# Kernel tuning notes

Measured on AMD Instinct MI355X. Metric: run time of the kernel, lower is better.

## Reference

```python
import jax, jax.numpy as jnp
import numpy as np

NUM_HEAD = 8
DIM_HEAD = 32
IN_DIM = 256  # = NUM_HEAD * DIM_HEAD
SLEN = 1024
BSZ = 8


def setup_inputs() -> dict:
    key = jax.random.key(0)
    ks = jax.random.split(key, 6)
    std = 1.0 / np.sqrt(DIM_HEAD).astype(np.float32)
    h = jax.random.normal(ks[0], (SLEN, BSZ, IN_DIM), dtype=jnp.float32)
    W_y = std * jax.random.normal(ks[1], (1, NUM_HEAD, DIM_HEAD, DIM_HEAD), dtype=jnp.float32)
    W_q = std * jax.random.normal(ks[2], (1, NUM_HEAD, DIM_HEAD, DIM_HEAD), dtype=jnp.float32)
    W_k = std * jax.random.normal(ks[3], (1, NUM_HEAD, DIM_HEAD, DIM_HEAD), dtype=jnp.float32)
    w_b = std * jax.random.normal(ks[4], (1, NUM_HEAD, DIM_HEAD, 4), dtype=jnp.float32)
    # out_linear: Linear(H*d -> in_dim, bias=False); torch weight shape (in_dim, H*d)
    W_out = jax.random.normal(ks[5], (IN_DIM, NUM_HEAD * DIM_HEAD), dtype=jnp.float32) / np.sqrt(NUM_HEAD * DIM_HEAD).astype(np.float32)
    return {"h": h, "W_y": W_y, "W_q": W_q, "W_k": W_k, "w_b": w_b, "W_out": W_out}


def _read(W, v):
    # W: (B,H,d,d), v: (B,H,d) -> (B,H,d)
    return jnp.einsum('bhij,bhj->bhi', W, v)


def _read_b(wb, v):
    # wb: (B,H,d,4), v: (B,H,d) -> (B,H,4)
    return jnp.einsum('bhik,bhi->bhk', wb, v)


def _srwm_forward(h, W_y, W_q, W_k, w_b, W_out):
    slen, bsz, _ = h.shape
    # reshape to heads and softmax the input (as in the torch forward)
    x = jax.nn.softmax(h.reshape(slen, bsz, NUM_HEAD, DIM_HEAD), axis=-1)  # (S,B,H,d)
    bc = lambda W: jnp.broadcast_to(W, (bsz,) + W.shape[1:])
    carry0 = (bc(W_y), bc(W_q), bc(W_k), bc(w_b))

    def step(carry, xt):
        Wy, Wq, Wk, wb = carry  # (B,H,d,d) x3, (B,H,d,4)
        yt = _read(Wy, xt)                                   # output read with current Wy
        qt = jax.nn.softmax(_read(Wq, xt), axis=-1)          # query
        kt = jax.nn.softmax(_read(Wk, xt), axis=-1)          # key
        bt = jax.nn.sigmoid(_read_b(wb, xt))                 # (B,H,4) learning rates
        # delta-rule self-referential update: W += beta * (W q - W k) (x) k
        dy = _read(Wy, qt) - _read(Wy, kt)
        dq = _read(Wq, qt) - _read(Wq, kt)
        dk = _read(Wk, qt) - _read(Wk, kt)
        db = _read_b(wb, qt) - _read_b(wb, kt)               # (B,H,4)
        outer = lambda u: u[..., :, None] * kt[..., None, :]
        Wy = Wy + bt[..., 0][..., None, None] * outer(dy)
        Wq = Wq + bt[..., 1][..., None, None] * outer(dq)
        Wk = Wk + bt[..., 2][..., None, None] * outer(dk)
        wb = wb + bt[..., 3][..., None, None] * (kt[..., :, None] * db[..., None, :])
        return (Wy, Wq, Wk, wb), yt

    _, ys = jax.lax.scan(step, carry0, x)                    # ys: (S,B,H,d)
    out = ys.reshape(slen, bsz, NUM_HEAD * DIM_HEAD) @ W_out.T  # (S,B,in_dim)
    return h + out  # dropout p=0 -> identity; residual


def reference(h, W_y, W_q, W_k, w_b, W_out):
    return _srwm_forward(h, W_y, W_q, W_k, w_b, W_out)
```

## Files before the change

### kernel.cpp

```cpp
#include <hip/hip_runtime.h>

#define DEV __device__ __forceinline__


template <int CTRL>
DEV float dppf(float x) {
  return __int_as_float(__builtin_amdgcn_update_dpp(
      0, __float_as_int(x), CTRL, 0xF, 0xF, true));
}

DEV float wsum32(float v) {
  v += dppf<0xB1>(v);
  v += dppf<0x4E>(v);
  v += dppf<0x141>(v);
  v += dppf<0x140>(v);
#if __has_builtin(__builtin_amdgcn_permlane16_swap)
  {
    auto p = __builtin_amdgcn_permlane16_swap(
        __float_as_uint(v), __float_as_uint(v), false, false);
    v = __uint_as_float(p[0]) + __uint_as_float(p[1]);
  }
#else
  v += __shfl_xor(v, 16, 64);
#endif
  return v;
}

DEV float halfsum(float v) {
#if __has_builtin(__builtin_amdgcn_permlane32_swap)
  auto p = __builtin_amdgcn_permlane32_swap(
      __float_as_uint(v), __float_as_uint(v), false, false);
  return __uint_as_float(p[0]) + __uint_as_float(p[1]);
#else
  return v + __shfl_xor(v, 32, 64);
#endif
}

#define SLEN 1024
#define NH 8
#define DH 32
#define HSTRIDE 2048


__global__ __launch_bounds__(256)
void srwm_xsm(const float* __restrict__ h, float* __restrict__ x) {
  int i = blockIdx.x * 256 + threadIdx.x;
  float e = __expf(h[i]);
  x[i] = __fdividef(e, wsum32(e));
}


#define BARRIER() \
  do { asm volatile("s_waitcnt lgkmcnt(0)" ::: "memory"); \
       __builtin_amdgcn_s_barrier(); } while (0)

#define REGION(T, P, XS, XP)                                                  \
  {                                                                           \
    \
    float ql[16], kl[16];                                                     \
    _Pragma("unroll") for (int j = 0; j < 16; j += 4) {                       \
      *(float4*)&ql[j] = *(const float4*)&qs[(P) ^ 1][c0 + j];                \
      *(float4*)&kl[j] = *(const float4*)&ks2[(P) ^ 1][c0 + j];               \
    }                                                                         \
    float Bw = bss[(P) ^ 1][w];                                               \
    _Pragma("unroll") for (int j = 0; j < 16; ++j) ql[j] -= kl[j];            \
                   \
    float d0 = 0.f, d1 = 0.f, d2 = 0.f, d3 = 0.f, s0 = 0.f, s1 = 0.f;        \
    _Pragma("unroll") for (int j = 0; j < 16; j += 4) {                       \
      d0 = fmaf(W[j],     ql[j],     d0);                                     \
      d1 = fmaf(W[j + 1], ql[j + 1], d1);                                     \
      d2 = fmaf(W[j + 2], ql[j + 2], d2);                                     \
      d3 = fmaf(W[j + 3], ql[j + 3], d3);                                     \
      s0 = fmaf(kl[j],     XS[j],     s0);                                    \
      s1 = fmaf(kl[j + 1], XS[j + 1], s1);                                    \
      s0 = fmaf(kl[j + 2], XS[j + 2], s0);                                    \
      s1 = fmaf(kl[j + 3], XS[j + 3], s1);                                    \
    }                                                                         \
    float dsum = halfsum((d0 + d1) + (d2 + d3));                              \
    float sv   = halfsum(s0 + s1);                                            \
        \
    int t2 = (T) + 2; if (t2 > SLEN - 1) t2 = SLEN - 1;                       \
    _Pragma("unroll") for (int j = 0; j < 16; j += 4)                         \
      *(float4*)&XS[j] = *(const float4*)(xb + (size_t)t2 * HSTRIDE + c0 + j);\
    float u  = Bw * dsum;                                                     \
    float aA = fmaf(u, sv, preA);                                             \
    if (w == 0) {                                                             \
      if (lane < DH) xb[(size_t)(T) * HSTRIDE + lane] = aA;          \
    } else if (w == 1) {                                                      \
      float e = __expf(aA); float qq = __fdividef(e, wsum32(e));              \
      qs[P][r] = qq;                         \
    } else if (w == 2) {                                                      \
      float e = __expf(aA); float kk2 = __fdividef(e, wsum32(e));             \
      ks2[P][r] = kk2;                                                        \
    } else {                                                                  \
      float sg = __fdividef(1.f, 1.f + __expf(-aA));                          \
      if (lane < 4) bss[P][lane] = sg;                                        \
    }                                                                         \
                                      \
    _Pragma("unroll") for (int j = 0; j < 16; ++j)                            \
      W[j] = fmaf(u, kl[j], W[j]);                                            \
    float p0 = 0.f, p1 = 0.f, p2 = 0.f, p3 = 0.f;                             \
    _Pragma("unroll") for (int j = 0; j < 16; j += 4) {                       \
      p0 = fmaf(W[j],     XP[j],     p0);                                     \
      p1 = fmaf(W[j + 1], XP[j + 1], p1);                                     \
      p2 = fmaf(W[j + 2], XP[j + 2], p2);                                     \
      p3 = fmaf(W[j + 3], XP[j + 3], p3);                                     \
    }                                                                         \
    preA = halfsum((p0 + p1) + (p2 + p3));                                    \
    BARRIER();                                                                \
  }

__global__ __launch_bounds__(256, 1)
void srwm_scan(const float* __restrict__ Wy0, const float* __restrict__ Wq0,
               const float* __restrict__ Wk0, const float* __restrict__ wb0,
               float* xy) {
  __shared__ float qs[2][DH];
  __shared__ float ks2[2][DH];
  __shared__ float bss[2][4];

  const int bh   = blockIdx.x;
  const int hd   = bh & 7;
  const int w    = threadIdx.x >> 6;
  const int lane = threadIdx.x & 63;
  const int r    = lane & 31;
  const int c0   = (lane >> 5) * 16;

  float W[16];
  if (w < 3) {
    const float* src = (w == 0) ? Wy0 : (w == 1) ? Wq0 : Wk0;
    const float* p = src + (hd * DH + r) * DH + c0;
#pragma unroll
    for (int j = 0; j < 16; j += 4) *(float4*)&W[j] = *(const float4*)(p + j);
  } else {
    const int kk = r & 3;
#pragma unroll
    for (int j = 0; j < 16; ++j) W[j] = wb0[(hd * DH + c0 + j) * 4 + kk];
  }

  if (threadIdx.x < DH) { qs[1][threadIdx.x] = 0.f; ks2[1][threadIdx.x] = 0.f; }
  if (threadIdx.x < 4)  { bss[1][threadIdx.x] = 0.f; bss[0][threadIdx.x] = 0.f; }

  float* xb = xy + bh * DH;

  float X0[16], X1[16];
#pragma unroll
  for (int j = 0; j < 16; j += 4) {
    *(float4*)&X0[j] = *(const float4*)(xb + c0 + j);
    *(float4*)&X1[j] = *(const float4*)(xb + HSTRIDE + c0 + j);
  }
  float p0 = 0.f, p1 = 0.f, p2 = 0.f, p3 = 0.f;
#pragma unroll
  for (int j = 0; j < 16; j += 4) {
    p0 = fmaf(W[j],     X0[j],     p0);
    p1 = fmaf(W[j + 1], X0[j + 1], p1);
    p2 = fmaf(W[j + 2], X0[j + 2], p2);
    p3 = fmaf(W[j + 3], X0[j + 3], p3);
  }
  float preA = halfsum((p0 + p1) + (p2 + p3));
  __syncthreads();

  for (int t = 0; t < SLEN; t += 2) {
    REGION(t,     0, X0, X1);
    REGION(t + 1, 1, X1, X0);
  }
}


__global__ __launch_bounds__(256)
void srwm_proj(const float* __restrict__ h, const float* __restrict__ ys,
               const float* __restrict__ Wout, float* __restrict__ out) {
  __shared__ float ytile[32][256];
  const int r0  = blockIdx.x * 32;
  const int tid = threadIdx.x;

  const float4* src = (const float4*)(ys + (size_t)r0 * 256);
  float4*       dst = (float4*)(&ytile[0][0]);
#pragma unroll
  for (int i = 0; i < 8; ++i) dst[tid + i * 256] = src[tid + i * 256];
  __syncthreads();

  float acc[32];
#pragma unroll
  for (int m = 0; m < 32; ++m) acc[m] = 0.f;

  const float* wrow = Wout + (size_t)tid * 256;
  for (int k = 0; k < 256; k += 4) {
    float4 w = *(const float4*)(wrow + k);
#pragma unroll
    for (int m = 0; m < 32; ++m) {
      float4 y4 = *(const float4*)(&ytile[m][k]);
      acc[m] = fmaf(w.x, y4.x,
               fmaf(w.y, y4.y,
               fmaf(w.z, y4.z,
               fmaf(w.w, y4.w, acc[m]))));
    }
  }

#pragma unroll
  for (int m = 0; m < 32; ++m) {
    int row = r0 + m;
    out[(size_t)row * 256 + tid] = h[(size_t)row * 256 + tid] + acc[m];
  }
}


extern "C" void kernel_launch(void* const* d_in, const int* in_sizes, int n_in,
                              void* d_out, int out_size, void* d_ws, size_t ws_size,
                              hipStream_t stream) {
  const float* h    = (const float*)d_in[0];
  const float* Wy0  = (const float*)d_in[1];
  const float* Wq0  = (const float*)d_in[2];
  const float* Wk0  = (const float*)d_in[3];
  const float* wb0  = (const float*)d_in[4];
  const float* Wout = (const float*)d_in[5];
  float* out = (float*)d_out;

  srwm_xsm <<<SLEN * HSTRIDE / 256, 256, 0, stream>>>(h, out);
  srwm_scan<<<64, 256, 0, stream>>>(Wy0, Wq0, Wk0, wb0, out);
  srwm_proj<<<256, 256, 0, stream>>>(h, out, Wout, out);
}
```

Before: 620.4 us.

## Split scan into producer wave for Wq/Wk/wb and consumer wave for Wy

The scan now uses 128 threads. One wave owns Wq, Wk and wb and computes q, k and beta each step. A second wave owns Wy and computes outputs, handing off through an LDS ring buffer with spin-wait counters in place of a block barrier each step. This takes the Wy work and its output stores off the recurrence critical path and drops the per-step s_barrier. It also uses packed v_pk_fma_f32 and ds_bpermute broadcasts. In exchange it relies on volatile LDS spin polling between waves for correctness and loses some parallelism per block.

```diff
diff --git a/kernel.cpp b/kernel.cpp
--- a/kernel.cpp
+++ b/kernel.cpp
@@ -2,6 +2,11 @@
 
 #define DEV __device__ __forceinline__
 
+typedef float f2 __attribute__((ext_vector_type(2)));
+
+DEV void pkfma(f2& acc, f2 a, f2 b) {
+  asm("v_pk_fma_f32 %0, %1, %2, %0" : "+v"(acc) : "v"(a), "v"(b));
+}
 
 template <int CTRL>
 DEV float dppf(float x) {
@@ -36,10 +41,16 @@
 #endif
 }
 
+DEV float rlane(float v, int l) {
+  return __int_as_float(__builtin_amdgcn_readlane(__float_as_int(v), l));
+}
+
 #define SLEN 1024
 #define NH 8
 #define DH 32
 #define HSTRIDE 2048
+#define RING 16
+#define SLOTF 72
 
 
 __global__ __launch_bounds__(256)
@@ -50,73 +61,108 @@
 }
 
 
-#define BARRIER() \
-  do { asm volatile("s_waitcnt lgkmcnt(0)" ::: "memory"); \
-       __builtin_amdgcn_s_barrier(); } while (0)
-
-#define REGION(T, P, XS, XP)                                                  \
+#define LOADX(DST, T)                                                         \
+  { const float* xp_ = xb + (size_t)(T) * HSTRIDE + c0;                       \
+    _Pragma("unroll") for (int q4 = 0; q4 < 4; ++q4) {                        \
+      float4 a_ = *(const float4*)(xp_ + q4 * 4);                             \
+      DST[2*q4] = f2{a_.x, a_.y}; DST[2*q4+1] = f2{a_.z, a_.w}; } }
+
+#define MV3(oq, ok, ob, V)                                                    \
+  { f2 aq0={0,0},aq1={0,0},ak0={0,0},ak1={0,0},ab0={0,0},ab1={0,0};           \
+    _Pragma("unroll") for (int j = 0; j < 8; j += 2) {                        \
+      pkfma(aq0, Wq2[j], V[j]); pkfma(aq1, Wq2[j+1], V[j+1]);                 \
+      pkfma(ak0, Wk2[j], V[j]); pkfma(ak1, Wk2[j+1], V[j+1]);                 \
+      pkfma(ab0, WB2[j], V[j]); pkfma(ab1, WB2[j+1], V[j+1]);                 \
+    }                                                                         \
+    f2 aq_=aq0+aq1, ak_=ak0+ak1, ab_=ab0+ab1;                                 \
+    oq = halfsum(aq_.x+aq_.y); ok = halfsum(ak_.x+ak_.y);                     \
+    ob = halfsum(ab_.x+ab_.y); }
+
+#define PSTEP(T, XC, XO)                                                      \
   {                                                                           \
-    \
-    float ql[16], kl[16];                                                     \
-    _Pragma("unroll") for (int j = 0; j < 16; j += 4) {                       \
-      *(float4*)&ql[j] = *(const float4*)&qs[(P) ^ 1][c0 + j];                \
-      *(float4*)&kl[j] = *(const float4*)&ks2[(P) ^ 1][c0 + j];               \
-    }                                                                         \
-    float Bw = bss[(P) ^ 1][w];                                               \
-    _Pragma("unroll") for (int j = 0; j < 16; ++j) ql[j] -= kl[j];            \
-                   \
-    float d0 = 0.f, d1 = 0.f, d2 = 0.f, d3 = 0.f, s0 = 0.f, s1 = 0.f;        \
-    _Pragma("unroll") for (int j = 0; j < 16; j += 4) {                       \
-      d0 = fmaf(W[j],     ql[j],     d0);                                     \
-      d1 = fmaf(W[j + 1], ql[j + 1], d1);                                     \
-      d2 = fmaf(W[j + 2], ql[j + 2], d2);                                     \
-      d3 = fmaf(W[j + 3], ql[j + 3], d3);                                     \
-      s0 = fmaf(kl[j],     XS[j],     s0);                                    \
-      s1 = fmaf(kl[j + 1], XS[j + 1], s1);                                    \
-      s0 = fmaf(kl[j + 2], XS[j + 2], s0);                                    \
-      s1 = fmaf(kl[j + 3], XS[j + 3], s1);                                    \
-    }                                                                         \
-    float dsum = halfsum((d0 + d1) + (d2 + d3));                              \
-    float sv   = halfsum(s0 + s1);                                            \
-        \
-    int t2 = (T) + 2; if (t2 > SLEN - 1) t2 = SLEN - 1;                       \
-    _Pragma("unroll") for (int j = 0; j < 16; j += 4)                         \
-      *(float4*)&XS[j] = *(const float4*)(xb + (size_t)t2 * HSTRIDE + c0 + j);\
-    float u  = Bw * dsum;                                                     \
-    float aA = fmaf(u, sv, preA);                                             \
-    if (w == 0) {                                                             \
-      if (lane < DH) xb[(size_t)(T) * HSTRIDE + lane] = aA;          \
-    } else if (w == 1) {                                                      \
-      float e = __expf(aA); float qq = __fdividef(e, wsum32(e));              \
-      qs[P][r] = qq;                         \
-    } else if (w == 2) {                                                      \
-      float e = __expf(aA); float kk2 = __fdividef(e, wsum32(e));             \
-      ks2[P][r] = kk2;                                                        \
-    } else {                                                                  \
-      float sg = __fdividef(1.f, 1.f + __expf(-aA));                          \
-      if (lane < 4) bss[P][lane] = sg;                                        \
+    int t2_ = (T) + 2; if (t2_ > SLEN - 1) t2_ = SLEN - 1;                    \
+    LOADX(XO, t2_);                         \
+    float eq_ = __expf(pAq), ek_ = __expf(pAk);                               \
+    float qv_ = __fdividef(eq_, wsum32(eq_));                                 \
+    float kv_ = __fdividef(ek_, wsum32(ek_));                                 \
+    float bs_ = __fdividef(1.f, 1.f + __expf(-pAb));                          \
+    float dvv_ = qv_ - kv_;                                                   \
+    f2 dvc[8], kc[8];                                                         \
+    _Pragma("unroll") for (int j = 0; j < 8; ++j) {                           \
+      f2 td_, tk_;                                                            \
+      td_.x = __int_as_float(__builtin_amdgcn_ds_bpermute(b4 + 8*j,     __float_as_int(dvv_))); \
+      td_.y = __int_as_float(__builtin_amdgcn_ds_bpermute(b4 + 8*j + 4, __float_as_int(dvv_))); \
+      tk_.x = __int_as_float(__builtin_amdgcn_ds_bpermute(b4 + 8*j,     __float_as_int(kv_))); \
+      tk_.y = __int_as_float(__builtin_amdgcn_ds_bpermute(b4 + 8*j + 4, __float_as_int(kv_))); \
+      dvc[j] = td_; kc[j] = tk_;                                              \
+    }                                                                         \
+    float dq_, dk_, db_;                                                      \
+    MV3(dq_, dk_, db_, dvc);                              \
+    float B1_ = rlane(bs_, 1), B2_ = rlane(bs_, 2), B3_ = rlane(bs_, 3);      \
+    float uq_ = B1_ * dq_, uk_ = B2_ * dk_, ub_ = B3_ * db_;                  \
+               \
+    float* sl_ = &ringf[((T) & (RING - 1)) * SLOTF];                          \
+    sl_[r] = dvv_; sl_[DH + r] = kv_;                                         \
+    if (lane == 0) sl_[2 * DH] = bs_;                                         \
+    __builtin_amdgcn_sched_barrier(0);                                        \
+    asm volatile("s_waitcnt lgkmcnt(0)");                                     \
+    __builtin_amdgcn_sched_barrier(0);                                        \
+    *pcv = (T) + 1;                                                           \
+    __builtin_amdgcn_sched_barrier(0);                                        \
+                                                      \
+    f2 uuq_ = f2{uq_, uq_}, uuk_ = f2{uk_, uk_}, uub_ = f2{ub_, ub_};         \
+    _Pragma("unroll") for (int j = 0; j < 8; ++j) {                           \
+      pkfma(Wq2[j], uuq_, kc[j]);                                             \
+      pkfma(Wk2[j], uuk_, kc[j]);                                             \
+      pkfma(WB2[j], uub_, kc[j]);                                             \
     }                                                                         \
                                       \
-    _Pragma("unroll") for (int j = 0; j < 16; ++j)                            \
-      W[j] = fmaf(u, kl[j], W[j]);                                            \
-    float p0 = 0.f, p1 = 0.f, p2 = 0.f, p3 = 0.f;                             \
-    _Pragma("unroll") for (int j = 0; j < 16; j += 4) {                       \
-      p0 = fmaf(W[j],     XP[j],     p0);                                     \
-      p1 = fmaf(W[j + 1], XP[j + 1], p1);                                     \
-      p2 = fmaf(W[j + 2], XP[j + 2], p2);                                     \
-      p3 = fmaf(W[j + 3], XP[j + 3], p3);                                     \
-    }                                                                         \
-    preA = halfsum((p0 + p1) + (p2 + p3));                                    \
-    BARRIER();                                                                \
-  }
-
-__global__ __launch_bounds__(256, 1)
+    MV3(pAq, pAk, pAb, XC);                                                   \
+                  \
+    if (((T) & (RING - 1)) == (RING - 1)) {                                   \
+      while (*ccv < (T) - (RING - 3)) {}                                      \
+    }                                                                         \
+  }
+
+#define CSTEP(T, XC)                                                          \
+  {                                                                           \
+    while (*pcv < (T) + 1) {}                                                 \
+    __builtin_amdgcn_sched_barrier(0);                                        \
+    const float* sl_ = &ringf[((T) & (RING - 1)) * SLOTF];                    \
+    f2 dvc[8], kc[8];                                                         \
+    _Pragma("unroll") for (int q4 = 0; q4 < 4; ++q4) {                        \
+      float4 a_ = *(const float4*)(sl_ + c0 + q4 * 4);                        \
+      dvc[2*q4] = f2{a_.x, a_.y}; dvc[2*q4+1] = f2{a_.z, a_.w};               \
+      float4 b_ = *(const float4*)(sl_ + DH + c0 + q4 * 4);                   \
+      kc[2*q4] = f2{b_.x, b_.y}; kc[2*q4+1] = f2{b_.z, b_.w};                 \
+    }                                                                         \
+    float B0_ = sl_[2 * DH];                                                  \
+    f2 a0_={0,0}, a1_={0,0};                                                  \
+    _Pragma("unroll") for (int j = 0; j < 8; j += 2) {                        \
+      pkfma(a0_, Wy2[j], XC[j]); pkfma(a1_, Wy2[j+1], XC[j+1]);               \
+    }                                                                         \
+    f2 as_ = a0_ + a1_; float yv_ = halfsum(as_.x + as_.y);                   \
+    if (lane < DH) xb[(size_t)(T) * HSTRIDE + lane] = yv_;                    \
+    int t2_ = (T) + 2; if (t2_ > SLEN - 1) t2_ = SLEN - 1;                    \
+    LOADX(XC, t2_);                         \
+    f2 d0_={0,0}, d1_={0,0};                                                  \
+    _Pragma("unroll") for (int j = 0; j < 8; j += 2) {                        \
+      pkfma(d0_, Wy2[j], dvc[j]); pkfma(d1_, Wy2[j+1], dvc[j+1]);             \
+    }                                                                         \
+    f2 ds_ = d0_ + d1_; float uy_ = B0_ * halfsum(ds_.x + ds_.y);             \
+    f2 uu_ = f2{uy_, uy_};                                                    \
+    _Pragma("unroll") for (int j = 0; j < 8; ++j) pkfma(Wy2[j], uu_, kc[j]);  \
+    __builtin_amdgcn_sched_barrier(0);                                        \
+    *ccv = (T) + 1;                                                           \
+    __builtin_amdgcn_sched_barrier(0);                                        \
+  }
+
+__global__ __launch_bounds__(128, 1)
 void srwm_scan(const float* __restrict__ Wy0, const float* __restrict__ Wq0,
                const float* __restrict__ Wk0, const float* __restrict__ wb0,
                float* xy) {
-  __shared__ float qs[2][DH];
-  __shared__ float ks2[2][DH];
-  __shared__ float bss[2][4];
+  __shared__ float ringf[RING * SLOTF];
+  __shared__ int pcnt, ccnt;
 
   const int bh   = blockIdx.x;
   const int hd   = bh & 7;
@@ -124,44 +170,64 @@
   const int lane = threadIdx.x & 63;
   const int r    = lane & 31;
   const int c0   = (lane >> 5) * 16;
-
-  float W[16];
-  if (w < 3) {
-    const float* src = (w == 0) ? Wy0 : (w == 1) ? Wq0 : Wk0;
-    const float* p = src + (hd * DH + r) * DH + c0;
-#pragma unroll
-    for (int j = 0; j < 16; j += 4) *(float4*)&W[j] = *(const float4*)(p + j);
+  const int b4   = c0 * 4;
+
+  volatile int* pcv = &pcnt;
+  volatile int* ccv = &ccnt;
+
+  if (threadIdx.x == 0) { pcnt = 0; ccnt = 0; }
+  __syncthreads();
+
+  float* xb = xy + bh * DH;
+
+  if (w == 0) {
+    f2 Wq2[8], Wk2[8], WB2[8];
+    {
+      const float* pq = Wq0 + (hd * DH + r) * DH + c0;
+      const float* pk = Wk0 + (hd * DH + r) * DH + c0;
+#pragma unroll
+      for (int q4 = 0; q4 < 4; ++q4) {
+        float4 a = *(const float4*)(pq + q4 * 4);
+        Wq2[2*q4] = f2{a.x, a.y}; Wq2[2*q4+1] = f2{a.z, a.w};
+        float4 b = *(const float4*)(pk + q4 * 4);
+        Wk2[2*q4] = f2{b.x, b.y}; Wk2[2*q4+1] = f2{b.z, b.w};
+      }
+      const int kk = r & 3;
+      float wbs[16];
+#pragma unroll
+      for (int j = 0; j < 16; ++j) wbs[j] = wb0[(hd * DH + c0 + j) * 4 + kk];
+#pragma unroll
+      for (int j = 0; j < 8; ++j) WB2[j] = f2{wbs[2*j], wbs[2*j+1]};
+    }
+
+    f2 XA[8], XB[8];
+    float pAq, pAk, pAb;
+    LOADX(XA, 0);
+    MV3(pAq, pAk, pAb, XA);
+    LOADX(XA, 1);
+
+    for (int t = 0; t < SLEN; t += 2) {
+      PSTEP(t,     XA, XB);
+      PSTEP(t + 1, XB, XA);
+    }
   } else {
-    const int kk = r & 3;
-#pragma unroll
-    for (int j = 0; j < 16; ++j) W[j] = wb0[(hd * DH + c0 + j) * 4 + kk];
-  }
-
-  if (threadIdx.x < DH) { qs[1][threadIdx.x] = 0.f; ks2[1][threadIdx.x] = 0.f; }
-  if (threadIdx.x < 4)  { bss[1][threadIdx.x] = 0.f; bss[0][threadIdx.x] = 0.f; }
-
-  float* xb = xy + bh * DH;
-
-  float X0[16], X1[16];
-#pragma unroll
-  for (int j = 0; j < 16; j += 4) {
-    *(float4*)&X0[j] = *(const float4*)(xb + c0 + j);
-    *(float4*)&X1[j] = *(const float4*)(xb + HSTRIDE + c0 + j);
-  }
-  float p0 = 0.f, p1 = 0.f, p2 = 0.f, p3 = 0.f;
-#pragma unroll
-  for (int j = 0; j < 16; j += 4) {
-    p0 = fmaf(W[j],     X0[j],     p0);
-    p1 = fmaf(W[j + 1], X0[j + 1], p1);
-    p2 = fmaf(W[j + 2], X0[j + 2], p2);
-    p3 = fmaf(W[j + 3], X0[j + 3], p3);
-  }
-  float preA = halfsum((p0 + p1) + (p2 + p3));
-  __syncthreads();
-
-  for (int t = 0; t < SLEN; t += 2) {
-    REGION(t,     0, X0, X1);
-    REGION(t + 1, 1, X1, X0);
+    f2 Wy2[8];
+    {
+      const float* py = Wy0 + (hd * DH + r) * DH + c0;
+#pragma unroll
+      for (int q4 = 0; q4 < 4; ++q4) {
+        float4 a = *(const float4*)(py + q4 * 4);
+        Wy2[2*q4] = f2{a.x, a.y}; Wy2[2*q4+1] = f2{a.z, a.w};
+      }
+    }
+    f2 XA[8], XB[8];
+    LOADX(XA, 0);
+    LOADX(XB, 1);
+
+    for (int t = 0; t < SLEN; t += 2) {
+      CSTEP(t,     XA);
+      CSTEP(t + 1, XB);
+    }
   }
 }
 
@@ -216,6 +282,6 @@
   float* out = (float*)d_out;
 
   srwm_xsm <<<SLEN * HSTRIDE / 256, 256, 0, stream>>>(h, out);
-  srwm_scan<<<64, 256, 0, stream>>>(Wy0, Wq0, Wk0, wb0, out);
+  srwm_scan<<<64, 128, 0, stream>>>(Wy0, Wq0, Wk0, wb0, out);
   srwm_proj<<<256, 256, 0, stream>>>(h, out, Wout, out);
 }
```

Result: slower. 806.1 us (+29.9%).
